# Kernel tuning notes

Hardware: AMD Instinct MI355X
Metric: run time of the kernel (lower is better)

The kernel has to match this reference:

```python
import jax, jax.numpy as jnp
import numpy as np

B, D, C = 256, 128, 8000
MARGIN = 0.5
SCALE = 64.0
EPS = 1e-12  # tf.nn.l2_normalize epsilon


def _l2_normalize(x, axis):
    # Matches tf.nn.l2_normalize: x * rsqrt(max(sum(x^2), eps))
    sq = jnp.sum(x * x, axis=axis, keepdims=True)
    return x * jax.lax.rsqrt(jnp.maximum(sq, EPS))


def setup_inputs() -> dict:
    key = jax.random.key(0)
    k1, k2, k3 = jax.random.split(key, 3)
    embds = jax.random.normal(k1, (B, D), dtype=jnp.float32)
    w = jax.random.normal(k2, (D, C), dtype=jnp.float32)
    labels = jax.random.randint(k3, (B,), 0, C, dtype=jnp.int32)
    return {"embds": embds, "w": w, "labels": labels}


def reference(embds, w, labels):
    normed_embds = _l2_normalize(embds, axis=1)          # [B, D]
    normed_w = _l2_normalize(w, axis=0)                  # [D, C]
    gr_w = normed_w.T[labels]                            # gather per-label columns -> [B, D]
    # dw[b, d, c] = gr_w[b, d] - normed_w[d, c]
    dw = gr_w[:, :, None] - normed_w[None, :, :]         # [B, D, C]
    normed_dw = _l2_normalize(dw, axis=1)                # normalize over feature dim D
    win = jnp.einsum('bd,bdc->bc', normed_embds, normed_dw)
    penalties = MARGIN - jnp.minimum(MARGIN, win)        # [B, C]
    cos_t = normed_embds @ normed_w                      # [B, C]
    logits = jax.nn.softmax(SCALE * cos_t, axis=-1)
    return (logits, penalties)
```

## Files before the change

kernel.cpp:

```cpp
#include <hip/hip_runtime.h>
#include <math.h>

#define BB 256
#define DD 128
#define CC 8000
#define EPSF 1e-12f
#define SCALEF 64.0f
#define MARGINF 0.5f

__global__ __launch_bounds__(256, 2) void fused_kernel(
    const float* __restrict__ embds, const float* __restrict__ w,
    const int* __restrict__ labels, float* __restrict__ out,
    float* __restrict__ psums) {
  __shared__ float neS[DD * 16];
  __shared__ float gS[DD * 16];
  __shared__ float s1S[16];
  __shared__ int labS[16];

  int tid = threadIdx.x;
  int c0 = blockIdx.x * 256;
  int r0 = blockIdx.y * 16;

  {
    int r = tid >> 4;
    int k = tid & 15;
    int row = r0 + r;
    int lab = labels[row];
    const float4* e4 = (const float4*)(embds + row * DD + k * 8);
    float4 ea = e4[0], eb = e4[1];
    float ev[8] = {ea.x, ea.y, ea.z, ea.w, eb.x, eb.y, eb.z, eb.w};
    float wl[8];
    float se = 0.f, sw = 0.f, sx = 0.f;
    #pragma unroll
    for (int i = 0; i < 8; ++i) {
      wl[i] = w[(k * 8 + i) * CC + lab];
      se = fmaf(ev[i], ev[i], se);
      sw = fmaf(wl[i], wl[i], sw);
      sx = fmaf(ev[i], wl[i], sx);
    }
    #pragma unroll
    for (int off = 1; off < 16; off <<= 1) {
      se += __shfl_xor(se, off, 64);
      sw += __shfl_xor(sw, off, 64);
      sx += __shfl_xor(sx, off, 64);
    }
    float rn = rsqrtf(fmaxf(se, EPSF));
    float rl = rsqrtf(fmaxf(sw, EPSF));
    #pragma unroll
    for (int i = 0; i < 8; ++i) {
      neS[(k * 8 + i) * 16 + r] = ev[i] * rn;
      gS[(k * 8 + i) * 16 + r] = wl[i] * rl;
    }
    if (k == 0) { s1S[r] = sx * rn * rl; labS[r] = lab; }
  }
  __syncthreads();

  int tx = tid & 63;
  int ty = tid >> 6;
  int c = c0 + tx * 4;
  bool cok = c < CC;
  const float4* w4 = (const float4*)w;
  int wbase = (c0 >> 2) + tx;

  float accC[4][4], accG[4][4], colsum[4];
  #pragma unroll
  for (int rr = 0; rr < 4; ++rr)
    #pragma unroll
    for (int j = 0; j < 4; ++j) { accC[rr][j] = 0.f; accG[rr][j] = 0.f; }
  #pragma unroll
  for (int j = 0; j < 4; ++j) colsum[j] = 0.f;

  #pragma unroll 8
  for (int d = 0; d < DD; ++d) {
    float4 wv = cok ? w4[d * (CC / 4) + wbase] : make_float4(0.f, 0.f, 0.f, 0.f);
    float4 a = *(const float4*)&neS[d * 16 + ty * 4];
    float4 g = *(const float4*)&gS[d * 16 + ty * 4];
    float av[4] = {a.x, a.y, a.z, a.w};
    float gv[4] = {g.x, g.y, g.z, g.w};
    float wj[4] = {wv.x, wv.y, wv.z, wv.w};
    #pragma unroll
    for (int j = 0; j < 4; ++j) colsum[j] = fmaf(wj[j], wj[j], colsum[j]);
    #pragma unroll
    for (int rr = 0; rr < 4; ++rr) {
      #pragma unroll
      for (int j = 0; j < 4; ++j) {
        accC[rr][j] = fmaf(av[rr], wj[j], accC[rr][j]);
        accG[rr][j] = fmaf(gv[rr], wj[j], accG[rr][j]);
      }
    }
  }

  float rcj[4];
  #pragma unroll
  for (int j = 0; j < 4; ++j) rcj[j] = rsqrtf(fmaxf(colsum[j], EPSF));

  float* pen_base = out + (size_t)BB * CC;
  #pragma unroll
  for (int rr = 0; rr < 4; ++rr) {
    int lr = ty * 4 + rr;
    int row = r0 + lr;
    float s1v = s1S[lr];
    int lab = labS[lr];
    float penv[4], eo[4];
    float psum = 0.f;
    #pragma unroll
    for (int j = 0; j < 4; ++j) {
      float cs = accC[rr][j] * rcj[j];
      float gw = accG[rr][j] * rcj[j];
      float win = (s1v - cs) * rsqrtf(fmaxf(2.f - 2.f * gw, EPSF));
      if (c + j == lab) win = 0.f;
      penv[j] = MARGINF - fminf(MARGINF, win);
      float e = cok ? __expf(SCALEF * cs) : 0.f;
      eo[j] = e;
      psum += e;
    }
    if (cok) {
      size_t o4 = (size_t)row * (CC / 4) + wbase;
      ((float4*)pen_base)[o4] = make_float4(penv[0], penv[1], penv[2], penv[3]);
      ((float4*)out)[o4] = make_float4(eo[0], eo[1], eo[2], eo[3]);
    }
    #pragma unroll
    for (int off = 1; off < 64; off <<= 1) psum += __shfl_xor(psum, off, 64);
    if (tx == 0) psums[row * 32 + blockIdx.x] = psum;
  }
}

__global__ __launch_bounds__(512) void scale_kernel(
    float* __restrict__ out, const float* __restrict__ psums) {
  __shared__ float invS;
  int r = blockIdx.x;
  int tid = threadIdx.x;
  if (tid < 64) {
    float p = (tid < 32) ? psums[r * 32 + tid] : 0.f;
    #pragma unroll
    for (int off = 1; off < 32; off <<= 1) p += __shfl_xor(p, off, 64);
    if (tid == 0) invS = 1.f / p;
  }
  __syncthreads();
  float inv = invS;
  float4* row = (float4*)out + (size_t)r * (CC / 4);
  #pragma unroll
  for (int k = 0; k < 4; ++k) {
    int i = tid + k * 512;
    if (i < CC / 4) {
      float4 v = row[i];
      row[i] = make_float4(v.x * inv, v.y * inv, v.z * inv, v.w * inv);
    }
  }
}

extern "C" void kernel_launch(void* const* d_in, const int* in_sizes, int n_in,
                              void* d_out, int out_size, void* d_ws, size_t ws_size,
                              hipStream_t stream) {
  const float* embds = (const float*)d_in[0];
  const float* w = (const float*)d_in[1];
  const int* labels = (const int*)d_in[2];
  float* out = (float*)d_out;
  float* psums = (float*)d_ws;

  dim3 gA(32, 16);
  fused_kernel<<<gA, 256, 0, stream>>>(embds, w, labels, out, psums);
  scale_kernel<<<256, 512, 0, stream>>>(out, psums);
}
```

Baseline: 93.81 us.

## Fuse softmax normalization into main kernel via grid-level row-group barrier

Drops the separate scale kernel. Each block keeps its exponentials in registers, publishes partial row sums, then waits on a per-row-group atomic counter until all 32 column blocks have arrived. It then reads the totals and writes the normalized softmax output once. This removes a second launch and a full read-modify-write pass over the logits. The cost is a spin barrier that relies on all 512 blocks being co-resident, plus a timeout guard that could yield wrong results if blocks are not co-resident.

```diff
diff --git a/kernel.cpp b/kernel.cpp
--- a/kernel.cpp
+++ b/kernel.cpp
@@ -8,6 +8,9 @@
 #define SCALEF 64.0f
 #define MARGINF 0.5f
 
+
+__device__ int g_arrive[16 * 16];
+
 __global__ __launch_bounds__(256, 2) void fused_kernel(
     const float* __restrict__ embds, const float* __restrict__ w,
     const int* __restrict__ labels, float* __restrict__ out,
@@ -15,6 +18,7 @@
   __shared__ float neS[DD * 16];
   __shared__ float gS[DD * 16];
   __shared__ float s1S[16];
+  __shared__ float invS[16];
   __shared__ int labS[16];
 
   int tid = threadIdx.x;
@@ -95,13 +99,14 @@
   for (int j = 0; j < 4; ++j) rcj[j] = rsqrtf(fmaxf(colsum[j], EPSF));
 
   float* pen_base = out + (size_t)BB * CC;
+  float eo[4][4];
   #pragma unroll
   for (int rr = 0; rr < 4; ++rr) {
     int lr = ty * 4 + rr;
     int row = r0 + lr;
     float s1v = s1S[lr];
     int lab = labS[lr];
-    float penv[4], eo[4];
+    float penv[4];
     float psum = 0.f;
     #pragma unroll
     for (int j = 0; j < 4; ++j) {
@@ -111,40 +116,58 @@
       if (c + j == lab) win = 0.f;
       penv[j] = MARGINF - fminf(MARGINF, win);
       float e = cok ? __expf(SCALEF * cs) : 0.f;
-      eo[j] = e;
+      eo[rr][j] = e;
       psum += e;
     }
     if (cok) {
       size_t o4 = (size_t)row * (CC / 4) + wbase;
       ((float4*)pen_base)[o4] = make_float4(penv[0], penv[1], penv[2], penv[3]);
-      ((float4*)out)[o4] = make_float4(eo[0], eo[1], eo[2], eo[3]);
     }
     #pragma unroll
     for (int off = 1; off < 64; off <<= 1) psum += __shfl_xor(psum, off, 64);
-    if (tx == 0) psums[row * 32 + blockIdx.x] = psum;
+    if (tx == 0)
+      __hip_atomic_store(&psums[row * 32 + blockIdx.x], psum,
+                         __ATOMIC_RELAXED, __HIP_MEMORY_SCOPE_AGENT);
   }
-}
 
-__global__ __launch_bounds__(512) void scale_kernel(
-    float* __restrict__ out, const float* __restrict__ psums) {
-  __shared__ float invS;
-  int r = blockIdx.x;
-  int tid = threadIdx.x;
-  if (tid < 64) {
-    float p = (tid < 32) ? psums[r * 32 + tid] : 0.f;
-    #pragma unroll
-    for (int off = 1; off < 32; off <<= 1) p += __shfl_xor(p, off, 64);
-    if (tid == 0) invS = 1.f / p;
+  __syncthreads();
+
+  if (tid == 0) {
+    int* ctr = &g_arrive[blockIdx.y * 16];
+    int old = __hip_atomic_fetch_add(ctr, 1, __ATOMIC_RELEASE,
+                                     __HIP_MEMORY_SCOPE_AGENT);
+    int target = ((old >> 5) << 5) + 32;
+    int guard = 0;
+    while (__hip_atomic_load(ctr, __ATOMIC_ACQUIRE,
+                             __HIP_MEMORY_SCOPE_AGENT) < target &&
+           ++guard < (1 << 22)) {
+      __builtin_amdgcn_s_sleep(4);
+    }
   }
   __syncthreads();
-  float inv = invS;
-  float4* row = (float4*)out + (size_t)r * (CC / 4);
-  #pragma unroll
-  for (int k = 0; k < 4; ++k) {
-    int i = tid + k * 512;
-    if (i < CC / 4) {
-      float4 v = row[i];
-      row[i] = make_float4(v.x * inv, v.y * inv, v.z * inv, v.w * inv);
+
+  {
+    int lr = tid >> 4;
+    int jj = (tid & 15) * 2;
+    float* pr = psums + (size_t)(r0 + lr) * 32 + jj;
+    float p2 =
+        __hip_atomic_load(&pr[0], __ATOMIC_RELAXED, __HIP_MEMORY_SCOPE_AGENT) +
+        __hip_atomic_load(&pr[1], __ATOMIC_RELAXED, __HIP_MEMORY_SCOPE_AGENT);
+    #pragma unroll
+    for (int off = 1; off < 16; off <<= 1) p2 += __shfl_xor(p2, off, 64);
+    if ((tid & 15) == 0) invS[lr] = 1.f / p2;
+  }
+  __syncthreads();
+
+  if (cok) {
+    #pragma unroll
+    for (int rr = 0; rr < 4; ++rr) {
+      int lr = ty * 4 + rr;
+      int row = r0 + lr;
+      float inv = invS[lr];
+      size_t o4 = (size_t)row * (CC / 4) + wbase;
+      ((float4*)out)[o4] = make_float4(eo[rr][0] * inv, eo[rr][1] * inv,
+                                       eo[rr][2] * inv, eo[rr][3] * inv);
     }
   }
 }
@@ -160,5 +183,4 @@
 
   dim3 gA(32, 16);
   fused_kernel<<<gA, 256, 0, stream>>>(embds, w, labels, out, psums);
-  scale_kernel<<<256, 512, 0, stream>>>(out, psums);
 }
```

Measured after the change: 113.6 us. +21.1%, slower.

## Halve row tile, double grid, prefetch W in 4-row chunks with row-major smem

Applied to the files above, without the earlier changes.

Each block now handles 8 rows instead of 16, and the grid doubles to 1024 blocks. Launch bounds rise to 4 waves per SIMD for more occupancy. The inner loop now walks D in chunks of 4, software-prefetching the next four W float4 rows into registers, and the shared embedding and gather tiles are stored row-major so they can be read as float4 along D. The aim is better latency hiding and parallelism, at the cost of W being read twice as often from global memory/L2 across row blocks.

```diff
diff --git a/kernel.cpp b/kernel.cpp
--- a/kernel.cpp
+++ b/kernel.cpp
@@ -8,49 +8,47 @@
 #define SCALEF 64.0f
 #define MARGINF 0.5f
 
-__global__ __launch_bounds__(256, 2) void fused_kernel(
+__global__ __launch_bounds__(256, 4) void fused_kernel(
     const float* __restrict__ embds, const float* __restrict__ w,
     const int* __restrict__ labels, float* __restrict__ out,
     float* __restrict__ psums) {
-  __shared__ float neS[DD * 16];
-  __shared__ float gS[DD * 16];
-  __shared__ float s1S[16];
-  __shared__ int labS[16];
+  __shared__ float neS[8][DD];
+  __shared__ float gS[8][DD];
+  __shared__ float s1S[8];
+  __shared__ int labS[8];
 
   int tid = threadIdx.x;
   int c0 = blockIdx.x * 256;
-  int r0 = blockIdx.y * 16;
+  int r0 = blockIdx.y * 8;
 
   {
-    int r = tid >> 4;
-    int k = tid & 15;
+    int r = tid >> 5;
+    int k = tid & 31;
     int row = r0 + r;
     int lab = labels[row];
-    const float4* e4 = (const float4*)(embds + row * DD + k * 8);
-    float4 ea = e4[0], eb = e4[1];
-    float ev[8] = {ea.x, ea.y, ea.z, ea.w, eb.x, eb.y, eb.z, eb.w};
-    float wl[8];
+    float4 e4 = *(const float4*)(embds + row * DD + k * 4);
+    float ev[4] = {e4.x, e4.y, e4.z, e4.w};
+    float wl[4];
     float se = 0.f, sw = 0.f, sx = 0.f;
     #pragma unroll
-    for (int i = 0; i < 8; ++i) {
-      wl[i] = w[(k * 8 + i) * CC + lab];
+    for (int i = 0; i < 4; ++i) {
+      wl[i] = w[(k * 4 + i) * CC + lab];
       se = fmaf(ev[i], ev[i], se);
       sw = fmaf(wl[i], wl[i], sw);
       sx = fmaf(ev[i], wl[i], sx);
     }
     #pragma unroll
-    for (int off = 1; off < 16; off <<= 1) {
+    for (int off = 1; off < 32; off <<= 1) {
       se += __shfl_xor(se, off, 64);
       sw += __shfl_xor(sw, off, 64);
       sx += __shfl_xor(sx, off, 64);
     }
     float rn = rsqrtf(fmaxf(se, EPSF));
     float rl = rsqrtf(fmaxf(sw, EPSF));
-    #pragma unroll
-    for (int i = 0; i < 8; ++i) {
-      neS[(k * 8 + i) * 16 + r] = ev[i] * rn;
-      gS[(k * 8 + i) * 16 + r] = wl[i] * rl;
-    }
+    *(float4*)&neS[r][k * 4] =
+        make_float4(ev[0] * rn, ev[1] * rn, ev[2] * rn, ev[3] * rn);
+    *(float4*)&gS[r][k * 4] =
+        make_float4(wl[0] * rl, wl[1] * rl, wl[2] * rl, wl[3] * rl);
     if (k == 0) { s1S[r] = sx * rn * rl; labS[r] = lab; }
   }
   __syncthreads();
@@ -61,33 +59,56 @@
   bool cok = c < CC;
   const float4* w4 = (const float4*)w;
   int wbase = (c0 >> 2) + tx;
+  int row0 = ty * 2;
 
-  float accC[4][4], accG[4][4], colsum[4];
+  float accC[2][4], accG[2][4], colsum[4];
   #pragma unroll
-  for (int rr = 0; rr < 4; ++rr)
+  for (int rr = 0; rr < 2; ++rr)
     #pragma unroll
     for (int j = 0; j < 4; ++j) { accC[rr][j] = 0.f; accG[rr][j] = 0.f; }
   #pragma unroll
   for (int j = 0; j < 4; ++j) colsum[j] = 0.f;
 
-  #pragma unroll 8
-  for (int d = 0; d < DD; ++d) {
-    float4 wv = cok ? w4[d * (CC / 4) + wbase] : make_float4(0.f, 0.f, 0.f, 0.f);
-    float4 a = *(const float4*)&neS[d * 16 + ty * 4];
-    float4 g = *(const float4*)&gS[d * 16 + ty * 4];
-    float av[4] = {a.x, a.y, a.z, a.w};
-    float gv[4] = {g.x, g.y, g.z, g.w};
-    float wj[4] = {wv.x, wv.y, wv.z, wv.w};
+  float4 wn[4];
+  #pragma unroll
+  for (int q = 0; q < 4; ++q)
+    wn[q] = cok ? w4[q * (CC / 4) + wbase] : make_float4(0.f, 0.f, 0.f, 0.f);
+
+  #pragma unroll 2
+  for (int dc = 0; dc < 32; ++dc) {
+    int d = dc * 4;
+    float wv[4][4];
     #pragma unroll
-    for (int j = 0; j < 4; ++j) colsum[j] = fmaf(wj[j], wj[j], colsum[j]);
+    for (int q = 0; q < 4; ++q) {
+      wv[q][0] = wn[q].x; wv[q][1] = wn[q].y;
+      wv[q][2] = wn[q].z; wv[q][3] = wn[q].w;
+    }
+    if (dc < 31) {
+      #pragma unroll
+      for (int q = 0; q < 4; ++q)
+        wn[q] = cok ? w4[(d + 4 + q) * (CC / 4) + wbase]
+                    : make_float4(0.f, 0.f, 0.f, 0.f);
+    }
+    float4 a0 = *(const float4*)&neS[row0][d];
+    float4 a1 = *(const float4*)&neS[row0 + 1][d];
+    float4 g0 = *(const float4*)&gS[row0][d];
+    float4 g1 = *(const float4*)&gS[row0 + 1][d];
+    float av[2][4] = {{a0.x, a0.y, a0.z, a0.w}, {a1.x, a1.y, a1.z, a1.w}};
+    float gv[2][4] = {{g0.x, g0.y, g0.z, g0.w}, {g1.x, g1.y, g1.z, g1.w}};
     #pragma unroll
-    for (int rr = 0; rr < 4; ++rr) {
+    for (int q = 0; q < 4; ++q)
       #pragma unroll
-      for (int j = 0; j < 4; ++j) {
-        accC[rr][j] = fmaf(av[rr], wj[j], accC[rr][j]);
-        accG[rr][j] = fmaf(gv[rr], wj[j], accG[rr][j]);
-      }
-    }
+      for (int j = 0; j < 4; ++j)
+        colsum[j] = fmaf(wv[q][j], wv[q][j], colsum[j]);
+    #pragma unroll
+    for (int rr = 0; rr < 2; ++rr)
+      #pragma unroll
+      for (int q = 0; q < 4; ++q)
+        #pragma unroll
+        for (int j = 0; j < 4; ++j) {
+          accC[rr][j] = fmaf(av[rr][q], wv[q][j], accC[rr][j]);
+          accG[rr][j] = fmaf(gv[rr][q], wv[q][j], accG[rr][j]);
+        }
   }
 
   float rcj[4];
@@ -96,8 +117,8 @@
 
   float* pen_base = out + (size_t)BB * CC;
   #pragma unroll
-  for (int rr = 0; rr < 4; ++rr) {
-    int lr = ty * 4 + rr;
+  for (int rr = 0; rr < 2; ++rr) {
+    int lr = row0 + rr;
     int row = r0 + lr;
     float s1v = s1S[lr];
     int lab = labS[lr];
@@ -158,7 +179,7 @@
   float* out = (float*)d_out;
   float* psums = (float*)d_ws;
 
-  dim3 gA(32, 16);
+  dim3 gA(32, 32);
   fused_kernel<<<gA, 256, 0, stream>>>(embds, w, labels, out, psums);
   scale_kernel<<<256, 512, 0, stream>>>(out, psums);
 }
```

Result: slower. 96.33 us (+2.7%).

## Stage w tiles in LDS via async global_load_lds double buffering

Applied to the files above, without the earlier changes.

The main loop now streams w through a double-buffered LDS tile, filled with direct global-to-LDS async loads, instead of reading w from global memory once per d inside the FMA loop. The embedding and label-column arrays are transposed to row-major so each thread reads float4 chunks over four d values at once. Occupancy is requested at 3 blocks per SM, and out-of-range columns are clamped rather than masked. The aim is to hide global load latency behind compute, at the cost of more LDS use and a barrier per tile.

```diff
diff --git a/kernel.cpp b/kernel.cpp
--- a/kernel.cpp
+++ b/kernel.cpp
@@ -8,18 +8,42 @@
 #define SCALEF 64.0f
 #define MARGINF 0.5f
 
-__global__ __launch_bounds__(256, 2) void fused_kernel(
+#define RT 16
+#define CT 256
+#define TD 16
+#define NT (DD / TD)
+
+
+typedef const __attribute__((address_space(1))) void* gas_t;
+typedef __attribute__((address_space(3))) void* las_t;
+
+__global__ __launch_bounds__(256, 3) void fused_kernel(
     const float* __restrict__ embds, const float* __restrict__ w,
     const int* __restrict__ labels, float* __restrict__ out,
     float* __restrict__ psums) {
-  __shared__ float neS[DD * 16];
-  __shared__ float gS[DD * 16];
-  __shared__ float s1S[16];
-  __shared__ int labS[16];
+  __shared__ float wS[2][TD][CT];
+  __shared__ float neS[RT][DD];
+  __shared__ float gS[RT][DD];
+  __shared__ float s1S[RT];
+  __shared__ int labS[RT];
 
   int tid = threadIdx.x;
-  int c0 = blockIdx.x * 256;
-  int r0 = blockIdx.y * 16;
+  int lane = tid & 63;
+  int ty = tid >> 6;
+  int c0 = blockIdx.x * CT;
+  int r0 = blockIdx.y * RT;
+
+  int cg = c0 + lane * 4;
+  if (cg > CC - 4) cg = CC - 4;
+
+  #pragma unroll
+  for (int q = 0; q < 4; ++q) {
+    int dl = ty * 4 + q;
+    __builtin_amdgcn_global_load_lds((gas_t)(w + (size_t)dl * CC + cg),
+                                     (las_t)(&wS[0][dl][0]), 16, 0, 0);
+    __builtin_amdgcn_global_load_lds((gas_t)(w + (size_t)(TD + dl) * CC + cg),
+                                     (las_t)(&wS[1][dl][0]), 16, 0, 0);
+  }
 
   {
     int r = tid >> 4;
@@ -46,58 +70,91 @@
     }
     float rn = rsqrtf(fmaxf(se, EPSF));
     float rl = rsqrtf(fmaxf(sw, EPSF));
-    #pragma unroll
-    for (int i = 0; i < 8; ++i) {
-      neS[(k * 8 + i) * 16 + r] = ev[i] * rn;
-      gS[(k * 8 + i) * 16 + r] = wl[i] * rl;
-    }
+    *(float4*)&neS[r][k * 8] =
+        make_float4(ev[0] * rn, ev[1] * rn, ev[2] * rn, ev[3] * rn);
+    *(float4*)&neS[r][k * 8 + 4] =
+        make_float4(ev[4] * rn, ev[5] * rn, ev[6] * rn, ev[7] * rn);
+    *(float4*)&gS[r][k * 8] =
+        make_float4(wl[0] * rl, wl[1] * rl, wl[2] * rl, wl[3] * rl);
+    *(float4*)&gS[r][k * 8 + 4] =
+        make_float4(wl[4] * rl, wl[5] * rl, wl[6] * rl, wl[7] * rl);
     if (k == 0) { s1S[r] = sx * rn * rl; labS[r] = lab; }
   }
   __syncthreads();
 
-  int tx = tid & 63;
-  int ty = tid >> 6;
-  int c = c0 + tx * 4;
+  int tx = lane;
+  int wcol = tx * 4;
+  int c = c0 + wcol;
   bool cok = c < CC;
-  const float4* w4 = (const float4*)w;
+  int row0 = ty * 4;
+
+  float accC[4][4], accG[4][4], colsum[4];
+  #pragma unroll
+  for (int rr = 0; rr < 4; ++rr)
+    #pragma unroll
+    for (int j = 0; j < 4; ++j) { accC[rr][j] = 0.f; accG[rr][j] = 0.f; }
+  #pragma unroll
+  for (int j = 0; j < 4; ++j) colsum[j] = 0.f;
+
+  #pragma unroll 2
+  for (int t = 0; t < NT; ++t) {
+    const float(*wT)[CT] = wS[t & 1];
+    #pragma unroll
+    for (int dc = 0; dc < 4; ++dc) {
+      int dl = dc * 4;
+      int d = t * TD + dl;
+      float4 w0 = *(const float4*)&wT[dl + 0][wcol];
+      float4 w1 = *(const float4*)&wT[dl + 1][wcol];
+      float4 w2 = *(const float4*)&wT[dl + 2][wcol];
+      float4 w3 = *(const float4*)&wT[dl + 3][wcol];
+      float wq[4][4] = {{w0.x, w0.y, w0.z, w0.w},
+                        {w1.x, w1.y, w1.z, w1.w},
+                        {w2.x, w2.y, w2.z, w2.w},
+                        {w3.x, w3.y, w3.z, w3.w}};
+      float av[4][4], gv[4][4];
+      #pragma unroll
+      for (int rr = 0; rr < 4; ++rr) {
+        float4 a = *(const float4*)&neS[row0 + rr][d];
+        float4 g = *(const float4*)&gS[row0 + rr][d];
+        av[rr][0] = a.x; av[rr][1] = a.y; av[rr][2] = a.z; av[rr][3] = a.w;
+        gv[rr][0] = g.x; gv[rr][1] = g.y; gv[rr][2] = g.z; gv[rr][3] = g.w;
+      }
+      #pragma unroll
+      for (int q = 0; q < 4; ++q)
+        #pragma unroll
+        for (int j = 0; j < 4; ++j)
+          colsum[j] = fmaf(wq[q][j], wq[q][j], colsum[j]);
+      #pragma unroll
+      for (int rr = 0; rr < 4; ++rr)
+        #pragma unroll
+        for (int q = 0; q < 4; ++q)
+          #pragma unroll
+          for (int j = 0; j < 4; ++j) {
+            accC[rr][j] = fmaf(av[rr][q], wq[q][j], accC[rr][j]);
+            accG[rr][j] = fmaf(gv[rr][q], wq[q][j], accG[rr][j]);
+          }
+    }
+    __syncthreads();
+    if (t + 2 < NT) {
+      #pragma unroll
+      for (int q = 0; q < 4; ++q) {
+        int dl = ty * 4 + q;
+        __builtin_amdgcn_global_load_lds(
+            (gas_t)(w + (size_t)((t + 2) * TD + dl) * CC + cg),
+            (las_t)(&wS[t & 1][dl][0]), 16, 0, 0);
+      }
+    }
+  }
+
+  float rcj[4];
+  #pragma unroll
+  for (int j = 0; j < 4; ++j) rcj[j] = rsqrtf(fmaxf(colsum[j], EPSF));
+
+  float* pen_base = out + (size_t)BB * CC;
   int wbase = (c0 >> 2) + tx;
-
-  float accC[4][4], accG[4][4], colsum[4];
-  #pragma unroll
-  for (int rr = 0; rr < 4; ++rr)
-    #pragma unroll
-    for (int j = 0; j < 4; ++j) { accC[rr][j] = 0.f; accG[rr][j] = 0.f; }
-  #pragma unroll
-  for (int j = 0; j < 4; ++j) colsum[j] = 0.f;
-
-  #pragma unroll 8
-  for (int d = 0; d < DD; ++d) {
-    float4 wv = cok ? w4[d * (CC / 4) + wbase] : make_float4(0.f, 0.f, 0.f, 0.f);
-    float4 a = *(const float4*)&neS[d * 16 + ty * 4];
-    float4 g = *(const float4*)&gS[d * 16 + ty * 4];
-    float av[4] = {a.x, a.y, a.z, a.w};
-    float gv[4] = {g.x, g.y, g.z, g.w};
-    float wj[4] = {wv.x, wv.y, wv.z, wv.w};
-    #pragma unroll
-    for (int j = 0; j < 4; ++j) colsum[j] = fmaf(wj[j], wj[j], colsum[j]);
-    #pragma unroll
-    for (int rr = 0; rr < 4; ++rr) {
-      #pragma unroll
-      for (int j = 0; j < 4; ++j) {
-        accC[rr][j] = fmaf(av[rr], wj[j], accC[rr][j]);
-        accG[rr][j] = fmaf(gv[rr], wj[j], accG[rr][j]);
-      }
-    }
-  }
-
-  float rcj[4];
-  #pragma unroll
-  for (int j = 0; j < 4; ++j) rcj[j] = rsqrtf(fmaxf(colsum[j], EPSF));
-
-  float* pen_base = out + (size_t)BB * CC;
   #pragma unroll
   for (int rr = 0; rr < 4; ++rr) {
-    int lr = ty * 4 + rr;
+    int lr = row0 + rr;
     int row = r0 + lr;
     float s1v = s1S[lr];
     int lab = labS[lr];
```

Measured after the change: 264.4 us. 2.82x slower.
